# Optimization experiments

Hardware: AMD Instinct MI355X
Metric: run time of the kernel (lower is better)

The kernel has to match this reference:

```python
import jax, jax.numpy as jnp
import numpy as np

B, C, H, W = 8, 384, 32, 32
NUM_HEADS = 8
HEAD_DIM = C // NUM_HEADS
HIDDEN = max(32, C // 2)


def setup_inputs() -> dict:
    key = jax.random.key(0)
    ks = jax.random.split(key, 6)
    s = lambda fan_in: 1.0 / np.sqrt(fan_in)
    return {
        "x": jax.random.normal(ks[0], (B, C, H, W), dtype=jnp.float32),
        "qkv_w": jax.random.normal(ks[1], (C, 3 * C), dtype=jnp.float32) * s(C),
        "qkv_b": jnp.zeros((3 * C,), dtype=jnp.float32),
        "proj_w": jax.random.normal(ks[2], (C, C), dtype=jnp.float32) * s(C),
        "proj_b": jnp.zeros((C,), dtype=jnp.float32),
        "mlp_w1": jax.random.normal(ks[3], (2, HIDDEN), dtype=jnp.float32) * s(2),
        "mlp_b1": jnp.zeros((HIDDEN,), dtype=jnp.float32),
        "mlp_w2": jax.random.normal(ks[4], (HIDDEN, NUM_HEADS), dtype=jnp.float32) * s(HIDDEN),
        "mlp_b2": jnp.zeros((NUM_HEADS,), dtype=jnp.float32),
    }


def _relative_bias(h, w, mlp_w1, mlp_b1, mlp_w2, mlp_b2):
    ch = jnp.arange(h, dtype=jnp.float32)
    cw = jnp.arange(w, dtype=jnp.float32)
    coords = jnp.stack(jnp.meshgrid(ch, cw, indexing="ij"), axis=-1).reshape(-1, 2)  # [N,2]
    rel = coords[:, None, :] - coords[None, :, :]  # [N,N,2]
    denom = jnp.array([max(h - 1, 1), max(w - 1, 1)], dtype=jnp.float32)
    rel = rel / denom
    hidden = jax.nn.gelu(rel @ mlp_w1 + mlp_b1, approximate=False)
    bias = hidden @ mlp_w2 + mlp_b2  # [N,N,heads]
    return jnp.transpose(bias, (2, 0, 1))  # [heads,N,N]


def reference(x, qkv_w, qkv_b, proj_w, proj_b, mlp_w1, mlp_b1, mlp_w2, mlp_b2):
    b, c, h, w = x.shape
    n = h * w
    tokens = x.reshape(b, c, n).transpose(0, 2, 1)  # [B,N,C]
    qkv = (tokens @ qkv_w + qkv_b).reshape(b, n, 3, NUM_HEADS, HEAD_DIM)
    qkv = jnp.transpose(qkv, (2, 0, 3, 1, 4))  # [3,B,h,N,d]
    q, k, v = qkv[0], qkv[1], qkv[2]
    scale = HEAD_DIM ** -0.5
    attn = jnp.einsum("bhnd,bhmd->bhnm", q * scale, k)
    attn = attn + _relative_bias(h, w, mlp_w1, mlp_b1, mlp_w2, mlp_b2)[None]
    attn = jax.nn.softmax(attn, axis=-1)
    out = jnp.einsum("bhnm,bhmd->bhnd", attn, v)
    out = out.transpose(0, 2, 1, 3).reshape(b, n, c)
    out = out @ proj_w + proj_b
    return out.transpose(0, 2, 1).reshape(b, c, h, w)
```

## Files before the change

kernel.cpp:

```cpp
#include <hip/hip_runtime.h>
#include <hip/hip_bf16.h>
#include <math.h>

#define BB 8
#define CC 384
#define NT 1024
#define NHEAD 8
#define HD 48
#define HIDDEN 192
#define THREEC 1152

typedef short short8 __attribute__((ext_vector_type(8)));
typedef short short4v __attribute__((ext_vector_type(4)));
typedef float f32x4 __attribute__((ext_vector_type(4)));
typedef unsigned int uint2v __attribute__((ext_vector_type(2)));
typedef unsigned int uint4v __attribute__((ext_vector_type(4)));

static __device__ __forceinline__ short bf16bits(float v) {
  __hip_bfloat16 h = __float2bfloat16(v);
  return *(short*)&h;
}
static __device__ __forceinline__ unsigned pk2(float a, float b) {
  return __builtin_amdgcn_perm(__float_as_uint(b) + 0x8000u,
                               __float_as_uint(a) + 0x8000u, 0x07060302u);
}
static __device__ __forceinline__ void lds_dma16(const void* g, void* l) {
  __builtin_amdgcn_global_load_lds((const __attribute__((address_space(1))) unsigned*)g,
                                   (__attribute__((address_space(3))) unsigned*)l, 16, 0, 0);
}
static __device__ __forceinline__ void pl16swap(unsigned& a, unsigned& b) {
  asm("v_permlane16_swap_b32 %0, %1" : "+v"(a), "+v"(b));
}

__global__ __launch_bounds__(256) void k_prep(
    const float* __restrict__ x, const float* __restrict__ qkv_w,
    const float* __restrict__ proj_w,
    const float* __restrict__ w1, const float* __restrict__ b1,
    const float* __restrict__ w2, const float* __restrict__ b2,
    __hip_bfloat16* __restrict__ xt, __hip_bfloat16* __restrict__ wtq,
    __hip_bfloat16* __restrict__ wtp, float* __restrict__ tab) {
  const int bid = blockIdx.x;
  const int tid = threadIdx.x;
  if (bid >= 3648) {
    int g = (bid - 3648) * 256 + tid;
    int p = g >> 3, jc = g & 7;
    if (p >= 63 * 63) return;
    float rh = (float)(p / 63 - 31) * (1.0f / 31.0f);
    float rw = (float)(p % 63 - 31) * (1.0f / 31.0f);
    float acc[8] = {0.f, 0.f, 0.f, 0.f, 0.f, 0.f, 0.f, 0.f};
    const int j0 = jc * 24;
#pragma unroll 4
    for (int j = j0; j < j0 + 24; j++) {
      float pre = fmaf(rh, w1[j], fmaf(rw, w1[HIDDEN + j], b1[j]));
      float gl = 0.5f * pre * (1.0f + erff(pre * 0.70710678118654752f));
#pragma unroll
      for (int h = 0; h < 8; h++) acc[h] = fmaf(gl, w2[j * 8 + h], acc[h]);
    }
#pragma unroll
    for (int msk = 1; msk <= 4; msk <<= 1)
#pragma unroll
      for (int h = 0; h < 8; h++) acc[h] += __shfl_xor(acc[h], msk);
    if (jc == 0) {
#pragma unroll
      for (int h = 0; h < 8; h++)
        tab[h * 3969 + p] = (acc[h] + b2[h]) * 1.4426950408889634f;
    }
    return;
  }
  const float* src;
  __hip_bfloat16* dst;
  int R, C, r0, c0;
  if (bid < 3072) {
    int zi = bid / 384, rem = bid % 384;
    R = 384; C = 1024;
    r0 = (rem / 32) * 32; c0 = (rem % 32) * 32;
    src = x + (size_t)zi * R * C;
    dst = xt + (size_t)zi * R * C;
  } else if (bid < 3504) {
    int i = bid - 3072;
    R = 384; C = 1152;
    r0 = (i / 36) * 32; c0 = (i % 36) * 32;
    src = qkv_w; dst = wtq;
  } else {
    int i = bid - 3504;
    R = 384; C = 384;
    r0 = (i / 12) * 32; c0 = (i % 12) * 32;
    src = proj_w; dst = wtp;
  }
  __shared__ float t[32][33];
#pragma unroll
  for (int e = 0; e < 4; e++) {
    int i = tid + e * 256;
    int r = i >> 5, c = i & 31;
    t[r][c] = src[(size_t)(r0 + r) * C + c0 + c];
  }
  __syncthreads();
#pragma unroll
  for (int e = 0; e < 4; e++) {
    int i = tid + e * 256;
    int c = i >> 5, r = i & 31;
    dst[(size_t)(c0 + c) * R + r0 + r] = __float2bfloat16(t[r][c]);
  }
}

__global__ __launch_bounds__(256) void k_qkv_mfma(
    const __hip_bfloat16* __restrict__ xt,
    const __hip_bfloat16* __restrict__ wtq,
    const float* __restrict__ qkv_b,
    __hip_bfloat16* __restrict__ Qb,
    __hip_bfloat16* __restrict__ Kb,
    __hip_bfloat16* __restrict__ Vt)
{
  __shared__ __align__(16) char smem[17408];
  short* As = (short*)smem;
  short* Bs = (short*)(smem + 8192);
  float* Vf = (float*)smem;
  const int n0 = blockIdx.x * 64;
  const int m0 = blockIdx.y * 64;
  const int tid = threadIdx.x;
  const int wv = tid >> 6, lane = tid & 63, quad = lane >> 4, lq = lane & 15;
  const int lrow = lane >> 3;
  const int gsw = ((lane & 7) ^ lrow) * 8;
  const int sw0 = (quad ^ (lq & 7)) * 8;
  const int sw1 = sw0 ^ 32;
  f32x4 acc[4];
#pragma unroll
  for (int nt = 0; nt < 4; nt++) acc[nt] = (f32x4){0.f, 0.f, 0.f, 0.f};
  for (int kk = 0; kk < CC; kk += 64) {
    __syncthreads();
    for (int c = wv; c < 16; c += 4) {
      if (c < 8)
        lds_dma16((const short*)xt + (size_t)(m0 + c * 8 + lrow) * 384 + kk + gsw,
                  smem + c * 1024);
      else
        lds_dma16((const short*)wtq + (size_t)(n0 + (c - 8) * 8 + lrow) * 384 + kk + gsw,
                  smem + 8192 + (c - 8) * 1024);
    }
    __syncthreads();
    short8 a0 = *(const short8*)(As + (wv * 16 + lq) * 64 + sw0);
    short8 a1 = *(const short8*)(As + (wv * 16 + lq) * 64 + sw1);
#pragma unroll
    for (int nt = 0; nt < 4; nt++) {
      acc[nt] = __builtin_amdgcn_mfma_f32_16x16x32_bf16(
          a0, *(const short8*)(Bs + (nt * 16 + lq) * 64 + sw0), acc[nt], 0, 0, 0);
      acc[nt] = __builtin_amdgcn_mfma_f32_16x16x32_bf16(
          a1, *(const short8*)(Bs + (nt * 16 + lq) * 64 + sw1), acc[nt], 0, 0, 0);
    }
  }
  __syncthreads();
  const float qscale = 0.14433756729740643f * 1.4426950408889634f;
  const float sc = (n0 < 384) ? qscale : 1.0f;
#pragma unroll
  for (int nt = 0; nt < 4; nt++) {
    float bias = qkv_b[n0 + nt * 16 + lq];
#pragma unroll
    for (int r = 0; r < 4; r++)
      Vf[(nt * 16 + lq) * 68 + wv * 16 + quad * 4 + r] = (acc[nt][r] + bias) * sc;
  }
  __syncthreads();
  if (n0 >= 768) {
    int ch = tid & 63, grp = tid >> 6;
    int cg = n0 - 768 + ch;
    int head = cg / 48, d = cg - head * 48;
    int b = m0 >> 10;
    int n = (m0 & 1023) + grp * 16;
    const float* src = Vf + ch * 68 + grp * 16;
    short o16[16];
#pragma unroll
    for (int k = 0; k < 16; k++) o16[k] = bf16bits(src[k]);
    short* dst = (short*)Vt + ((size_t)(b * 8 + head) * 48 + d) * 1024 + n;
    *(short8*)dst = *(short8*)o16;
    *(short8*)(dst + 8) = *(short8*)(o16 + 8);
  } else {
    const int which = n0 >= 384;
    short* Out = which ? (short*)Kb : (short*)Qb;
    int n_l = tid & 63, seg = tid >> 6;
    int rr0 = (n0 - which * 384) + seg * 16;
    int head = rr0 / 48, d0 = rr0 - head * 48;
    int b = m0 >> 10;
    int n_g = (m0 & 1023) + n_l;
    const float* src = Vf + (seg * 16) * 68 + n_l;
    short o16[16];
#pragma unroll
    for (int k = 0; k < 16; k++) o16[k] = bf16bits(src[k * 68]);
    short* dst = Out + (((size_t)(b * 8 + head) << 10) + n_g) * 64 + d0;
    *(short8*)dst = *(short8*)o16;
    *(short8*)(dst + 8) = *(short8*)(o16 + 8);
    if (d0 == 0) {
      short8 z = (short8){0, 0, 0, 0, 0, 0, 0, 0};
      *(short8*)(dst + 48) = z;
      *(short8*)(dst + 56) = z;
    }
  }
}

#define K0_OFF 0
#define K1_OFF 8192
#define V0_OFF 16384
#define V1_OFF 22528
#define TR_OFF 28672
#define SMEM_SZ 30720
__global__ __launch_bounds__(256, 4) void k_flash(
    const __hip_bfloat16* __restrict__ Qb, const __hip_bfloat16* __restrict__ Kb,
    const __hip_bfloat16* __restrict__ Vt, const float* __restrict__ tab,
    __hip_bfloat16* __restrict__ ATb)
{
  __shared__ __align__(16) char smem[SMEM_SZ];
  float* Os = (float*)smem;

  const int tid = threadIdx.x;
  const int wv = tid >> 6, lane = tid & 63, quad = lane >> 4, lq = lane & 15;
  const int bh = blockIdx.x;
  const int q0 = blockIdx.y * 64;
  const int b = bh >> 3, h = bh & 7;
  const int inr0 = q0 >> 5;

  const int nrow = q0 + wv * 16 + lq;
  const int jnr = nrow & 31;
  const int rloc = (nrow >> 5) - inr0 + 1;
  const int tbase = rloc * 63 + jnr + 31 - 4 * quad;

  short8 qf0, qf1;
  {
    const short* qp = (const short*)Qb + ((size_t)(bh << 10) + nrow) * 64;
    qf0 = *(const short8*)(qp + quad * 8);
    qf1 = *(const short8*)(qp + 32 + quad * 8);
  }
  short8 onesv;
#pragma unroll
  for (int j = 0; j < 8; j++) onesv[j] = (short)0x3F80;

  f32x4 O[4];
#pragma unroll
  for (int dt = 0; dt < 4; dt++) O[dt] = (f32x4){0.f, 0.f, 0.f, 0.f};

  const short* kgp = (const short*)Kb + ((size_t)(bh << 10)) * 64;
  const short* vgp = (const short*)Vt + (size_t)bh * 48 * 1024;
  const float* tabg = tab + h * 3969;
  const int lrow = lane >> 3;
  const int gsw = ((lane & 7) ^ lrow) * 8;
  const int sw0 = (quad ^ (lq & 7)) * 8;
  const int sw1 = sw0 ^ 32;
  const int vq = ((quad & 1) << 1) | (quad >> 1);
  const int swv0 = (vq ^ (lq & 7)) * 8;
  const int swv1 = swv0 ^ 32;

  for (int c = wv; c < 15; c += 4) {
    if (c < 8)
      lds_dma16(kgp + (size_t)(c * 8 + lrow) * 64 + gsw, smem + K0_OFF + c * 1024);
    else if (c < 14)
      lds_dma16(vgp + (size_t)((c - 8) * 8 + lrow) * 1024 + gsw,
                smem + V0_OFF + (c - 8) * 1024);
    else
      lds_dma16(tabg + (inr0 + 30) * 63 + lane * 4, smem + TR_OFF);
  }

  for (int it = 0; it < 16; it++) {
    const int m0 = it * 64;
    const int buf = it & 1;
    __syncthreads();
    if (it < 15) {
      const int nbuf = buf ^ 1;
      const int mn = m0 + 64;
      for (int c = wv; c < 15; c += 4) {
        if (c < 8)
          lds_dma16(kgp + (size_t)(mn + c * 8 + lrow) * 64 + gsw,
                    smem + K0_OFF + nbuf * 8192 + c * 1024);
        else if (c < 14)
          lds_dma16(vgp + (size_t)((c - 8) * 8 + lrow) * 1024 + mn + gsw,
                    smem + V0_OFF + nbuf * 6144 + (c - 8) * 1024);
        else
          lds_dma16(tabg + (inr0 + 28 - 2 * it) * 63 + lane * 4,
                    smem + TR_OFF + nbuf * 1024);
      }
    }
    const short* Kl = (const short*)(smem + K0_OFF + buf * 8192);
    const short* Vl = (const short*)(smem + V0_OFF + buf * 6144);
    const float* Tl = (const float*)(smem + TR_OFF + buf * 1024);

    float s[4][4];
    __builtin_amdgcn_s_setprio(1);
#pragma unroll
    for (int nt = 0; nt < 4; nt++) {
      const float* tn = Tl + tbase - (nt >= 2 ? 63 : 0) - (nt & 1) * 16;
      f32x4 c;
      c[0] = tn[0]; c[1] = tn[-1]; c[2] = tn[-2]; c[3] = tn[-3];
      c = __builtin_amdgcn_mfma_f32_16x16x32_bf16(
          *(const short8*)(Kl + (nt * 16 + lq) * 64 + sw0), qf0, c, 0, 0, 0);
      c = __builtin_amdgcn_mfma_f32_16x16x32_bf16(
          *(const short8*)(Kl + (nt * 16 + lq) * 64 + sw1), qf1, c, 0, 0, 0);
#pragma unroll
      for (int r = 0; r < 4; r++) s[nt][r] = c[r];
    }
    __builtin_amdgcn_s_setprio(0);
#pragma unroll
    for (int nt = 0; nt < 4; nt++)
#pragma unroll
      for (int r = 0; r < 4; r++) s[nt][r] = exp2f(s[nt][r]);
    uint4v p0, p1;
    {
      unsigned a, bb_;
      a = pk2(s[0][0], s[0][1]); bb_ = pk2(s[1][0], s[1][1]);
      pl16swap(a, bb_); p0[0] = a; p0[2] = bb_;
      a = pk2(s[0][2], s[0][3]); bb_ = pk2(s[1][2], s[1][3]);
      pl16swap(a, bb_); p0[1] = a; p0[3] = bb_;
      a = pk2(s[2][0], s[2][1]); bb_ = pk2(s[3][0], s[3][1]);
      pl16swap(a, bb_); p1[0] = a; p1[2] = bb_;
      a = pk2(s[2][2], s[2][3]); bb_ = pk2(s[3][2], s[3][3]);
      pl16swap(a, bb_); p1[1] = a; p1[3] = bb_;
    }
    short8 pf0 = *(short8*)&p0;
    short8 pf1 = *(short8*)&p1;
    __builtin_amdgcn_s_setprio(1);
#pragma unroll
    for (int dt = 0; dt < 3; dt++)
      O[dt] = __builtin_amdgcn_mfma_f32_16x16x32_bf16(
          *(const short8*)(Vl + (dt * 16 + lq) * 64 + swv0), pf0, O[dt], 0, 0, 0);
    O[3] = __builtin_amdgcn_mfma_f32_16x16x32_bf16(onesv, pf0, O[3], 0, 0, 0);
#pragma unroll
    for (int dt = 0; dt < 3; dt++)
      O[dt] = __builtin_amdgcn_mfma_f32_16x16x32_bf16(
          *(const short8*)(Vl + (dt * 16 + lq) * 64 + swv1), pf1, O[dt], 0, 0, 0);
    O[3] = __builtin_amdgcn_mfma_f32_16x16x32_bf16(onesv, pf1, O[3], 0, 0, 0);
    __builtin_amdgcn_s_setprio(0);
  }
  float inv = 1.0f / O[3][0];
  __syncthreads();
#pragma unroll
  for (int dt = 0; dt < 3; dt++)
#pragma unroll
    for (int r = 0; r < 4; r++)
      Os[(wv * 16 + lq) * 52 + dt * 16 + quad * 4 + r] = O[dt][r] * inv;
  __syncthreads();
  {
    int row = tid >> 2, cg = (tid & 3) * 12;
    const float* src = Os + row * 52 + cg;
    short outp[12];
#pragma unroll
    for (int k = 0; k < 12; k++) outp[k] = bf16bits(src[k]);
    short* dst = (short*)ATb + ((size_t)(b << 10) + q0 + row) * 384 + h * 48 + cg;
    *(short4v*)dst = *(short4v*)outp;
    *(short4v*)(dst + 4) = *(short4v*)(outp + 4);
    *(short4v*)(dst + 8) = *(short4v*)(outp + 8);
  }
}

__global__ __launch_bounds__(256) void k_proj_mfma(
    const __hip_bfloat16* __restrict__ ATb,
    const __hip_bfloat16* __restrict__ wtp,
    const float* __restrict__ pb, float* __restrict__ out) {
  __shared__ __align__(16) char smem[16384];
  short* As = (short*)smem;
  short* Bs = (short*)(smem + 8192);
  const int c0 = blockIdx.x * 64;
  const int n0 = blockIdx.y * 64;
  const int b = blockIdx.z;
  const int tid = threadIdx.x;
  const int wv = tid >> 6, lane = tid & 63, quad = lane >> 4, lq = lane & 15;
  const int lrow = lane >> 3;
  const int gsw = ((lane & 7) ^ lrow) * 8;
  const int sw0 = (quad ^ (lq & 7)) * 8;
  const int sw1 = sw0 ^ 32;
  f32x4 acc[4];
#pragma unroll
  for (int nt = 0; nt < 4; nt++) acc[nt] = (f32x4){0.f, 0.f, 0.f, 0.f};
  for (int kk = 0; kk < CC; kk += 64) {
    __syncthreads();
    for (int c = wv; c < 16; c += 4) {
      if (c < 8)
        lds_dma16((const short*)wtp + (size_t)(c0 + c * 8 + lrow) * 384 + kk + gsw,
                  smem + c * 1024);
      else
        lds_dma16((const short*)ATb + ((size_t)(b << 10) + n0 + (c - 8) * 8 + lrow) * 384 + kk + gsw,
                  smem + 8192 + (c - 8) * 1024);
    }
    __syncthreads();
    short8 a0 = *(const short8*)(As + (wv * 16 + lq) * 64 + sw0);
    short8 a1 = *(const short8*)(As + (wv * 16 + lq) * 64 + sw1);
#pragma unroll
    for (int nt = 0; nt < 4; nt++) {
      acc[nt] = __builtin_amdgcn_mfma_f32_16x16x32_bf16(
          a0, *(const short8*)(Bs + (nt * 16 + lq) * 64 + sw0), acc[nt], 0, 0, 0);
      acc[nt] = __builtin_amdgcn_mfma_f32_16x16x32_bf16(
          a1, *(const short8*)(Bs + (nt * 16 + lq) * 64 + sw1), acc[nt], 0, 0, 0);
    }
  }
#pragma unroll
  for (int nt = 0; nt < 4; nt++) {
    int n = n0 + nt * 16 + lq;
#pragma unroll
    for (int r = 0; r < 4; r++) {
      int c = c0 + wv * 16 + quad * 4 + r;
      out[((size_t)b * 384 + c) * 1024 + n] = acc[nt][r] + pb[c];
    }
  }
}

extern "C" void kernel_launch(void* const* d_in, const int* in_sizes, int n_in,
                              void* d_out, int out_size, void* d_ws, size_t ws_size,
                              hipStream_t stream) {
  const float* x = (const float*)d_in[0];
  const float* qkv_w = (const float*)d_in[1];
  const float* qkv_b = (const float*)d_in[2];
  const float* proj_w = (const float*)d_in[3];
  const float* proj_b = (const float*)d_in[4];
  const float* w1 = (const float*)d_in[5];
  const float* b1 = (const float*)d_in[6];
  const float* w2 = (const float*)d_in[7];
  const float* b2 = (const float*)d_in[8];
  float* out = (float*)d_out;

  char* w = (char*)d_ws;
  __hip_bfloat16* xt = (__hip_bfloat16*)w;   w += (size_t)8192 * 384 * 2;
  __hip_bfloat16* wtq = (__hip_bfloat16*)w;  w += (size_t)1152 * 384 * 2;
  __hip_bfloat16* wtp = (__hip_bfloat16*)w;  w += (size_t)384 * 384 * 2;
  __hip_bfloat16* Qb = (__hip_bfloat16*)w;   w += (size_t)64 * 1024 * 64 * 2;
  __hip_bfloat16* Kb = (__hip_bfloat16*)w;   w += (size_t)64 * 1024 * 64 * 2;
  __hip_bfloat16* Vt = (__hip_bfloat16*)w;   w += (size_t)64 * 48 * 1024 * 2;
  __hip_bfloat16* ATb = (__hip_bfloat16*)w;  w += (size_t)8192 * 384 * 2;
  float* tab = (float*)w;                    w += (size_t)8 * 3969 * 4 + 1024;

  k_prep<<<dim3(3773), dim3(256), 0, stream>>>(x, qkv_w, proj_w, w1, b1, w2, b2,
                                               xt, wtq, wtp, tab);
  k_qkv_mfma<<<dim3(18, 128), dim3(256), 0, stream>>>(xt, wtq, qkv_b, Qb, Kb, Vt);
  k_flash<<<dim3(64, 16), dim3(256), 0, stream>>>(Qb, Kb, Vt, tab, ATb);
  k_proj_mfma<<<dim3(6, 16, 8), dim3(256), 0, stream>>>(ATb, wtp, proj_b, out);
}
```

Baseline: 166.8 us.

## Split flash attention over key halves and read V straight into registers

The flash kernel now splits the 1024 keys into two halves along a new grid z dimension. Each half writes unnormalized fp32 partial outputs and row sums to a workspace, and a new combine kernel adds them, normalizes and writes bf16. V fragments are loaded directly from global memory into registers instead of being staged in LDS. This cuts LDS use and raises the occupancy hint to 6 blocks per CU, doubling the number of blocks for better CU fill. In exchange it adds an extra kernel launch, about 25MB of fp32 partial traffic, and uncoalesced-ish global V loads on the critical path. Partial sums can be added without rescaling because no running max is used.

```diff
diff --git a/kernel.cpp b/kernel.cpp
--- a/kernel.cpp
+++ b/kernel.cpp
@@ -196,23 +196,23 @@
 
 #define K0_OFF 0
 #define K1_OFF 8192
-#define V0_OFF 16384
-#define V1_OFF 22528
-#define TR_OFF 28672
-#define SMEM_SZ 30720
-__global__ __launch_bounds__(256, 4) void k_flash(
+#define TR_OFF 16384
+#define SMEM_SZ 18432
+__global__ __launch_bounds__(256, 6) void k_flash(
     const __hip_bfloat16* __restrict__ Qb, const __hip_bfloat16* __restrict__ Kb,
     const __hip_bfloat16* __restrict__ Vt, const float* __restrict__ tab,
-    __hip_bfloat16* __restrict__ ATb)
+    float* __restrict__ Opart,
+    float* __restrict__ Lpart)
 {
   __shared__ __align__(16) char smem[SMEM_SZ];
-  float* Os = (float*)smem;
 
   const int tid = threadIdx.x;
   const int wv = tid >> 6, lane = tid & 63, quad = lane >> 4, lq = lane & 15;
   const int bh = blockIdx.x;
   const int q0 = blockIdx.y * 64;
-  const int b = bh >> 3, h = bh & 7;
+  const int z = blockIdx.z;
+  const int kt0 = z * 8;
+  const int h = bh & 7;
   const int inr0 = q0 >> 5;
 
   const int nrow = q0 + wv * 16 + lq;
@@ -242,40 +242,44 @@
   const int sw0 = (quad ^ (lq & 7)) * 8;
   const int sw1 = sw0 ^ 32;
   const int vq = ((quad & 1) << 1) | (quad >> 1);
-  const int swv0 = (vq ^ (lq & 7)) * 8;
-  const int swv1 = swv0 ^ 32;
-
-  for (int c = wv; c < 15; c += 4) {
+
+  for (int c = wv; c < 9; c += 4) {
     if (c < 8)
-      lds_dma16(kgp + (size_t)(c * 8 + lrow) * 64 + gsw, smem + K0_OFF + c * 1024);
-    else if (c < 14)
-      lds_dma16(vgp + (size_t)((c - 8) * 8 + lrow) * 1024 + gsw,
-                smem + V0_OFF + (c - 8) * 1024);
+      lds_dma16(kgp + (size_t)(kt0 * 64 + c * 8 + lrow) * 64 + gsw,
+                smem + K0_OFF + c * 1024);
     else
-      lds_dma16(tabg + (inr0 + 30) * 63 + lane * 4, smem + TR_OFF);
-  }
-
-  for (int it = 0; it < 16; it++) {
-    const int m0 = it * 64;
+      lds_dma16(tabg + (inr0 + 30 - 2 * kt0) * 63 + lane * 4, smem + TR_OFF);
+  }
+
+  for (int it = 0; it < 8; it++) {
+    const int kt = kt0 + it;
+    const int m0 = kt * 64;
     const int buf = it & 1;
     __syncthreads();
-    if (it < 15) {
+
+    short8 vf0[3], vf1[3];
+    {
+      const short* vp = vgp + (size_t)lq * 1024 + m0 + vq * 8;
+#pragma unroll
+      for (int dt = 0; dt < 3; dt++) {
+        vf0[dt] = *(const short8*)(vp + dt * 16384);
+        vf1[dt] = *(const short8*)(vp + dt * 16384 + 32);
+      }
+    }
+
+    if (it < 7) {
       const int nbuf = buf ^ 1;
       const int mn = m0 + 64;
-      for (int c = wv; c < 15; c += 4) {
+      for (int c = wv; c < 9; c += 4) {
         if (c < 8)
           lds_dma16(kgp + (size_t)(mn + c * 8 + lrow) * 64 + gsw,
                     smem + K0_OFF + nbuf * 8192 + c * 1024);
-        else if (c < 14)
-          lds_dma16(vgp + (size_t)((c - 8) * 8 + lrow) * 1024 + mn + gsw,
-                    smem + V0_OFF + nbuf * 6144 + (c - 8) * 1024);
         else
-          lds_dma16(tabg + (inr0 + 28 - 2 * it) * 63 + lane * 4,
+          lds_dma16(tabg + (inr0 + 28 - 2 * kt) * 63 + lane * 4,
                     smem + TR_OFF + nbuf * 1024);
       }
     }
     const short* Kl = (const short*)(smem + K0_OFF + buf * 8192);
-    const short* Vl = (const short*)(smem + V0_OFF + buf * 6144);
     const float* Tl = (const float*)(smem + TR_OFF + buf * 1024);
 
     float s[4][4];
@@ -314,35 +318,45 @@
     __builtin_amdgcn_s_setprio(1);
 #pragma unroll
     for (int dt = 0; dt < 3; dt++)
-      O[dt] = __builtin_amdgcn_mfma_f32_16x16x32_bf16(
-          *(const short8*)(Vl + (dt * 16 + lq) * 64 + swv0), pf0, O[dt], 0, 0, 0);
+      O[dt] = __builtin_amdgcn_mfma_f32_16x16x32_bf16(vf0[dt], pf0, O[dt], 0, 0, 0);
     O[3] = __builtin_amdgcn_mfma_f32_16x16x32_bf16(onesv, pf0, O[3], 0, 0, 0);
 #pragma unroll
     for (int dt = 0; dt < 3; dt++)
-      O[dt] = __builtin_amdgcn_mfma_f32_16x16x32_bf16(
-          *(const short8*)(Vl + (dt * 16 + lq) * 64 + swv1), pf1, O[dt], 0, 0, 0);
+      O[dt] = __builtin_amdgcn_mfma_f32_16x16x32_bf16(vf1[dt], pf1, O[dt], 0, 0, 0);
     O[3] = __builtin_amdgcn_mfma_f32_16x16x32_bf16(onesv, pf1, O[3], 0, 0, 0);
     __builtin_amdgcn_s_setprio(0);
   }
-  float inv = 1.0f / O[3][0];
-  __syncthreads();
-#pragma unroll
-  for (int dt = 0; dt < 3; dt++)
-#pragma unroll
-    for (int r = 0; r < 4; r++)
-      Os[(wv * 16 + lq) * 52 + dt * 16 + quad * 4 + r] = O[dt][r] * inv;
-  __syncthreads();
   {
-    int row = tid >> 2, cg = (tid & 3) * 12;
-    const float* src = Os + row * 52 + cg;
-    short outp[12];
-#pragma unroll
-    for (int k = 0; k < 12; k++) outp[k] = bf16bits(src[k]);
-    short* dst = (short*)ATb + ((size_t)(b << 10) + q0 + row) * 384 + h * 48 + cg;
-    *(short4v*)dst = *(short4v*)outp;
-    *(short4v*)(dst + 4) = *(short4v*)(outp + 4);
-    *(short4v*)(dst + 8) = *(short4v*)(outp + 8);
-  }
+    const int q = q0 + wv * 16 + lq;
+    float* op = Opart + (((size_t)(z * 64 + bh) << 10) + q) * 48 + quad * 4;
+#pragma unroll
+    for (int dt = 0; dt < 3; dt++) *(f32x4*)(op + dt * 16) = O[dt];
+    if (quad == 0) Lpart[((size_t)(z * 64 + bh) << 10) + q] = O[3][0];
+  }
+}
+
+__global__ __launch_bounds__(256) void k_comb(
+    const float* __restrict__ Opart, const float* __restrict__ Lpart,
+    __hip_bfloat16* __restrict__ ATb) {
+  const int bh = blockIdx.x, b = bh >> 3, h = bh & 7;
+  const int q = blockIdx.y * 64 + (threadIdx.x >> 2);
+  const int cg = (threadIdx.x & 3) * 12;
+  const size_t r0 = (((size_t)bh << 10) + q) * 48 + cg;
+  const size_t r1 = (((size_t)(64 + bh) << 10) + q) * 48 + cg;
+  const float inv = 1.0f / (Lpart[((size_t)bh << 10) + q] +
+                            Lpart[(size_t)65536 + ((size_t)bh << 10) + q]);
+  short outp[12];
+#pragma unroll
+  for (int g = 0; g < 3; g++) {
+    f32x4 a = *(const f32x4*)(Opart + r0 + g * 4);
+    f32x4 c = *(const f32x4*)(Opart + r1 + g * 4);
+#pragma unroll
+    for (int r = 0; r < 4; r++) outp[g * 4 + r] = bf16bits((a[r] + c[r]) * inv);
+  }
+  short* dst = (short*)ATb + (((size_t)b << 10) + q) * 384 + h * 48 + cg;
+  *(short4v*)dst = *(short4v*)outp;
+  *(short4v*)(dst + 4) = *(short4v*)(outp + 4);
+  *(short4v*)(dst + 8) = *(short4v*)(outp + 8);
 }
 
 __global__ __launch_bounds__(256) void k_proj_mfma(
@@ -419,10 +433,13 @@
   __hip_bfloat16* Vt = (__hip_bfloat16*)w;   w += (size_t)64 * 48 * 1024 * 2;
   __hip_bfloat16* ATb = (__hip_bfloat16*)w;  w += (size_t)8192 * 384 * 2;
   float* tab = (float*)w;                    w += (size_t)8 * 3969 * 4 + 1024;
+  float* Opart = (float*)w;                  w += (size_t)2 * 64 * 1024 * 48 * 4;
+  float* Lpart = (float*)w;                  w += (size_t)2 * 64 * 1024 * 4;
 
   k_prep<<<dim3(3773), dim3(256), 0, stream>>>(x, qkv_w, proj_w, w1, b1, w2, b2,
                                                xt, wtq, wtp, tab);
   k_qkv_mfma<<<dim3(18, 128), dim3(256), 0, stream>>>(xt, wtq, qkv_b, Qb, Kb, Vt);
-  k_flash<<<dim3(64, 16), dim3(256), 0, stream>>>(Qb, Kb, Vt, tab, ATb);
+  k_flash<<<dim3(64, 16, 2), dim3(256), 0, stream>>>(Qb, Kb, Vt, tab, Opart, Lpart);
+  k_comb<<<dim3(64, 16), dim3(256), 0, stream>>>(Opart, Lpart, ATb);
   k_proj_mfma<<<dim3(6, 16, 8), dim3(256), 0, stream>>>(ATb, wtp, proj_b, out);
 }
```

Result: slower. 207.0 us (+24.1%).

## Load V fragments directly from a tiled global layout into registers

Applied to the files above, without the earlier changes.

The QKV kernel now writes V in a per-64-key-tile blocked layout, so each flash-attention tile's V block is contiguous. The flash kernel loads its V MFMA operands straight from global memory into registers instead of DMA-staging them through double-buffered LDS. This shrinks LDS use from about 30 KB to 18 KB per block and removes the V LDS reads. In exchange every wave re-reads V from global or L2 on each iteration, with load latency exposed right before the PV MFMAs and only partly hidden.

```diff
diff --git a/kernel.cpp b/kernel.cpp
--- a/kernel.cpp
+++ b/kernel.cpp
@@ -109,7 +109,7 @@
     const float* __restrict__ qkv_b,
     __hip_bfloat16* __restrict__ Qb,
     __hip_bfloat16* __restrict__ Kb,
-    __hip_bfloat16* __restrict__ Vt)
+    __hip_bfloat16* __restrict__ Vr)
 {
   __shared__ __align__(16) char smem[17408];
   short* As = (short*)smem;
@@ -163,12 +163,12 @@
     int cg = n0 - 768 + ch;
     int head = cg / 48, d = cg - head * 48;
     int b = m0 >> 10;
-    int n = (m0 & 1023) + grp * 16;
+    int kt = (m0 & 1023) >> 6;
     const float* src = Vf + ch * 68 + grp * 16;
     short o16[16];
 #pragma unroll
     for (int k = 0; k < 16; k++) o16[k] = bf16bits(src[k]);
-    short* dst = (short*)Vt + ((size_t)(b * 8 + head) * 48 + d) * 1024 + n;
+    short* dst = (short*)Vr + ((((size_t)(b * 8 + head) * 16 + kt) * 48 + d) << 6) + grp * 16;
     *(short8*)dst = *(short8*)o16;
     *(short8*)(dst + 8) = *(short8*)(o16 + 8);
   } else {
@@ -195,14 +195,11 @@
 }
 
 #define K0_OFF 0
-#define K1_OFF 8192
-#define V0_OFF 16384
-#define V1_OFF 22528
-#define TR_OFF 28672
-#define SMEM_SZ 30720
+#define TR_OFF 16384
+#define SMEM_SZ 18432
 __global__ __launch_bounds__(256, 4) void k_flash(
     const __hip_bfloat16* __restrict__ Qb, const __hip_bfloat16* __restrict__ Kb,
-    const __hip_bfloat16* __restrict__ Vt, const float* __restrict__ tab,
+    const __hip_bfloat16* __restrict__ Vr, const float* __restrict__ tab,
     __hip_bfloat16* __restrict__ ATb)
 {
   __shared__ __align__(16) char smem[SMEM_SZ];
@@ -235,47 +232,48 @@
   for (int dt = 0; dt < 4; dt++) O[dt] = (f32x4){0.f, 0.f, 0.f, 0.f};
 
   const short* kgp = (const short*)Kb + ((size_t)(bh << 10)) * 64;
-  const short* vgp = (const short*)Vt + (size_t)bh * 48 * 1024;
+  const short* vgp = (const short*)Vr + (size_t)bh * 49152;
   const float* tabg = tab + h * 3969;
   const int lrow = lane >> 3;
   const int gsw = ((lane & 7) ^ lrow) * 8;
   const int sw0 = (quad ^ (lq & 7)) * 8;
   const int sw1 = sw0 ^ 32;
   const int vq = ((quad & 1) << 1) | (quad >> 1);
-  const int swv0 = (vq ^ (lq & 7)) * 8;
-  const int swv1 = swv0 ^ 32;
-
-  for (int c = wv; c < 15; c += 4) {
+
+  for (int c = wv; c < 9; c += 4) {
     if (c < 8)
       lds_dma16(kgp + (size_t)(c * 8 + lrow) * 64 + gsw, smem + K0_OFF + c * 1024);
-    else if (c < 14)
-      lds_dma16(vgp + (size_t)((c - 8) * 8 + lrow) * 1024 + gsw,
-                smem + V0_OFF + (c - 8) * 1024);
     else
       lds_dma16(tabg + (inr0 + 30) * 63 + lane * 4, smem + TR_OFF);
   }
 
   for (int it = 0; it < 16; it++) {
-    const int m0 = it * 64;
     const int buf = it & 1;
     __syncthreads();
+
+    short8 vf0[3], vf1[3];
+    {
+      const short* vp = vgp + it * 3072 + lq * 64 + vq * 8;
+#pragma unroll
+      for (int dt = 0; dt < 3; dt++) {
+        vf0[dt] = *(const short8*)(vp + dt * 1024);
+        vf1[dt] = *(const short8*)(vp + dt * 1024 + 32);
+      }
+    }
+
     if (it < 15) {
       const int nbuf = buf ^ 1;
-      const int mn = m0 + 64;
-      for (int c = wv; c < 15; c += 4) {
+      const int mn = (it + 1) * 64;
+      for (int c = wv; c < 9; c += 4) {
         if (c < 8)
           lds_dma16(kgp + (size_t)(mn + c * 8 + lrow) * 64 + gsw,
                     smem + K0_OFF + nbuf * 8192 + c * 1024);
-        else if (c < 14)
-          lds_dma16(vgp + (size_t)((c - 8) * 8 + lrow) * 1024 + mn + gsw,
-                    smem + V0_OFF + nbuf * 6144 + (c - 8) * 1024);
         else
           lds_dma16(tabg + (inr0 + 28 - 2 * it) * 63 + lane * 4,
                     smem + TR_OFF + nbuf * 1024);
       }
     }
     const short* Kl = (const short*)(smem + K0_OFF + buf * 8192);
-    const short* Vl = (const short*)(smem + V0_OFF + buf * 6144);
     const float* Tl = (const float*)(smem + TR_OFF + buf * 1024);
 
     float s[4][4];
@@ -314,13 +312,11 @@
     __builtin_amdgcn_s_setprio(1);
 #pragma unroll
     for (int dt = 0; dt < 3; dt++)
-      O[dt] = __builtin_amdgcn_mfma_f32_16x16x32_bf16(
-          *(const short8*)(Vl + (dt * 16 + lq) * 64 + swv0), pf0, O[dt], 0, 0, 0);
+      O[dt] = __builtin_amdgcn_mfma_f32_16x16x32_bf16(vf0[dt], pf0, O[dt], 0, 0, 0);
     O[3] = __builtin_amdgcn_mfma_f32_16x16x32_bf16(onesv, pf0, O[3], 0, 0, 0);
 #pragma unroll
     for (int dt = 0; dt < 3; dt++)
-      O[dt] = __builtin_amdgcn_mfma_f32_16x16x32_bf16(
-          *(const short8*)(Vl + (dt * 16 + lq) * 64 + swv1), pf1, O[dt], 0, 0, 0);
+      O[dt] = __builtin_amdgcn_mfma_f32_16x16x32_bf16(vf1[dt], pf1, O[dt], 0, 0, 0);
     O[3] = __builtin_amdgcn_mfma_f32_16x16x32_bf16(onesv, pf1, O[3], 0, 0, 0);
     __builtin_amdgcn_s_setprio(0);
   }
@@ -416,13 +412,13 @@
   __hip_bfloat16* wtp = (__hip_bfloat16*)w;  w += (size_t)384 * 384 * 2;
   __hip_bfloat16* Qb = (__hip_bfloat16*)w;   w += (size_t)64 * 1024 * 64 * 2;
   __hip_bfloat16* Kb = (__hip_bfloat16*)w;   w += (size_t)64 * 1024 * 64 * 2;
-  __hip_bfloat16* Vt = (__hip_bfloat16*)w;   w += (size_t)64 * 48 * 1024 * 2;
+  __hip_bfloat16* Vr = (__hip_bfloat16*)w;   w += (size_t)64 * 16 * 48 * 64 * 2;
   __hip_bfloat16* ATb = (__hip_bfloat16*)w;  w += (size_t)8192 * 384 * 2;
   float* tab = (float*)w;                    w += (size_t)8 * 3969 * 4 + 1024;
 
   k_prep<<<dim3(3773), dim3(256), 0, stream>>>(x, qkv_w, proj_w, w1, b1, w2, b2,
                                                xt, wtq, wtp, tab);
-  k_qkv_mfma<<<dim3(18, 128), dim3(256), 0, stream>>>(xt, wtq, qkv_b, Qb, Kb, Vt);
-  k_flash<<<dim3(64, 16), dim3(256), 0, stream>>>(Qb, Kb, Vt, tab, ATb);
+  k_qkv_mfma<<<dim3(18, 128), dim3(256), 0, stream>>>(xt, wtq, qkv_b, Qb, Kb, Vr);
+  k_flash<<<dim3(64, 16), dim3(256), 0, stream>>>(Qb, Kb, Vr, tab, ATb);
   k_proj_mfma<<<dim3(6, 16, 8), dim3(256), 0, stream>>>(ATb, wtp, proj_b, out);
 }
```

New measurement: 182.0 us. +9.1%, slower.

## Double-buffer LDS DMA tiles in QKV and projection GEMM kernels

Applied to the files above, without the earlier changes.

The QKV and output-projection MFMA GEMMs now double-buffer their shared-memory tiles. The first K tile is prefetched before the loop, and each iteration issues the global-to-LDS DMA for the next tile into the alternate buffer before computing on the current one. This removes one barrier per iteration and overlaps load latency with MFMA work. It also raises wave priority around the MFMA block with s_setprio. LDS per block grows to 32 KB, which may lower occupancy per CU.

```diff
diff --git a/kernel.cpp b/kernel.cpp
--- a/kernel.cpp
+++ b/kernel.cpp
@@ -111,9 +111,7 @@
     __hip_bfloat16* __restrict__ Kb,
     __hip_bfloat16* __restrict__ Vt)
 {
-  __shared__ __align__(16) char smem[17408];
-  short* As = (short*)smem;
-  short* Bs = (short*)(smem + 8192);
+  __shared__ __align__(16) char smem[32768];
   float* Vf = (float*)smem;
   const int n0 = blockIdx.x * 64;
   const int m0 = blockIdx.y * 64;
@@ -126,19 +124,34 @@
   f32x4 acc[4];
 #pragma unroll
   for (int nt = 0; nt < 4; nt++) acc[nt] = (f32x4){0.f, 0.f, 0.f, 0.f};
-  for (int kk = 0; kk < CC; kk += 64) {
+  for (int c = wv; c < 16; c += 4) {
+    if (c < 8)
+      lds_dma16((const short*)xt + (size_t)(m0 + c * 8 + lrow) * 384 + gsw,
+                smem + c * 1024);
+    else
+      lds_dma16((const short*)wtq + (size_t)(n0 + (c - 8) * 8 + lrow) * 384 + gsw,
+                smem + 8192 + (c - 8) * 1024);
+  }
+  for (int t = 0; t < 6; t++) {
+    const int bo = (t & 1) << 14;
     __syncthreads();
-    for (int c = wv; c < 16; c += 4) {
-      if (c < 8)
-        lds_dma16((const short*)xt + (size_t)(m0 + c * 8 + lrow) * 384 + kk + gsw,
-                  smem + c * 1024);
-      else
-        lds_dma16((const short*)wtq + (size_t)(n0 + (c - 8) * 8 + lrow) * 384 + kk + gsw,
-                  smem + 8192 + (c - 8) * 1024);
-    }
-    __syncthreads();
+    if (t < 5) {
+      const int no = bo ^ 16384;
+      const int kk = (t + 1) * 64;
+      for (int c = wv; c < 16; c += 4) {
+        if (c < 8)
+          lds_dma16((const short*)xt + (size_t)(m0 + c * 8 + lrow) * 384 + kk + gsw,
+                    smem + no + c * 1024);
+        else
+          lds_dma16((const short*)wtq + (size_t)(n0 + (c - 8) * 8 + lrow) * 384 + kk + gsw,
+                    smem + no + 8192 + (c - 8) * 1024);
+      }
+    }
+    const short* As = (const short*)(smem + bo);
+    const short* Bs = (const short*)(smem + bo + 8192);
     short8 a0 = *(const short8*)(As + (wv * 16 + lq) * 64 + sw0);
     short8 a1 = *(const short8*)(As + (wv * 16 + lq) * 64 + sw1);
+    __builtin_amdgcn_s_setprio(1);
 #pragma unroll
     for (int nt = 0; nt < 4; nt++) {
       acc[nt] = __builtin_amdgcn_mfma_f32_16x16x32_bf16(
@@ -146,6 +159,7 @@
       acc[nt] = __builtin_amdgcn_mfma_f32_16x16x32_bf16(
           a1, *(const short8*)(Bs + (nt * 16 + lq) * 64 + sw1), acc[nt], 0, 0, 0);
     }
+    __builtin_amdgcn_s_setprio(0);
   }
   __syncthreads();
   const float qscale = 0.14433756729740643f * 1.4426950408889634f;
@@ -349,9 +363,7 @@
     const __hip_bfloat16* __restrict__ ATb,
     const __hip_bfloat16* __restrict__ wtp,
     const float* __restrict__ pb, float* __restrict__ out) {
-  __shared__ __align__(16) char smem[16384];
-  short* As = (short*)smem;
-  short* Bs = (short*)(smem + 8192);
+  __shared__ __align__(16) char smem[32768];
   const int c0 = blockIdx.x * 64;
   const int n0 = blockIdx.y * 64;
   const int b = blockIdx.z;
@@ -364,19 +376,34 @@
   f32x4 acc[4];
 #pragma unroll
   for (int nt = 0; nt < 4; nt++) acc[nt] = (f32x4){0.f, 0.f, 0.f, 0.f};
-  for (int kk = 0; kk < CC; kk += 64) {
+  for (int c = wv; c < 16; c += 4) {
+    if (c < 8)
+      lds_dma16((const short*)wtp + (size_t)(c0 + c * 8 + lrow) * 384 + gsw,
+                smem + c * 1024);
+    else
+      lds_dma16((const short*)ATb + ((size_t)(b << 10) + n0 + (c - 8) * 8 + lrow) * 384 + gsw,
+                smem + 8192 + (c - 8) * 1024);
+  }
+  for (int t = 0; t < 6; t++) {
+    const int bo = (t & 1) << 14;
     __syncthreads();
-    for (int c = wv; c < 16; c += 4) {
-      if (c < 8)
-        lds_dma16((const short*)wtp + (size_t)(c0 + c * 8 + lrow) * 384 + kk + gsw,
-                  smem + c * 1024);
-      else
-        lds_dma16((const short*)ATb + ((size_t)(b << 10) + n0 + (c - 8) * 8 + lrow) * 384 + kk + gsw,
-                  smem + 8192 + (c - 8) * 1024);
-    }
-    __syncthreads();
+    if (t < 5) {
+      const int no = bo ^ 16384;
+      const int kk = (t + 1) * 64;
+      for (int c = wv; c < 16; c += 4) {
+        if (c < 8)
+          lds_dma16((const short*)wtp + (size_t)(c0 + c * 8 + lrow) * 384 + kk + gsw,
+                    smem + no + c * 1024);
+        else
+          lds_dma16((const short*)ATb + ((size_t)(b << 10) + n0 + (c - 8) * 8 + lrow) * 384 + kk + gsw,
+                    smem + no + 8192 + (c - 8) * 1024);
+      }
+    }
+    const short* As = (const short*)(smem + bo);
+    const short* Bs = (const short*)(smem + bo + 8192);
     short8 a0 = *(const short8*)(As + (wv * 16 + lq) * 64 + sw0);
     short8 a1 = *(const short8*)(As + (wv * 16 + lq) * 64 + sw1);
+    __builtin_amdgcn_s_setprio(1);
 #pragma unroll
     for (int nt = 0; nt < 4; nt++) {
       acc[nt] = __builtin_amdgcn_mfma_f32_16x16x32_bf16(
@@ -384,6 +411,7 @@
       acc[nt] = __builtin_amdgcn_mfma_f32_16x16x32_bf16(
           a1, *(const short8*)(Bs + (nt * 16 + lq) * 64 + sw1), acc[nt], 0, 0, 0);
     }
+    __builtin_amdgcn_s_setprio(0);
   }
 #pragma unroll
   for (int nt = 0; nt < 4; nt++) {
```

After: 169.3 us. No clear change (+1.5%).
